# Performance work log

Hardware: AMD Instinct MI355X
Metric: run time of the kernel (lower is better)

Reference implementation:

```python
import jax, jax.numpy as jnp
import numpy as np

N_NODES = 100000


def _graph_conv(x, W, b, src, dst, norm):
    # DGL GraphConv(norm='left'): scale source features by 1/out_degree,
    # aggregate (sum over incoming edges). in_feats > out_feats so weight
    # multiply happens before aggregation (mathematically equivalent either way).
    h = x @ W  # [N, out]
    msg = (h * norm[:, None])[src]  # gather per-edge messages [E, out]
    agg = jax.ops.segment_sum(msg, dst, num_segments=N_NODES)
    return agg + b


def setup_inputs() -> dict:
    key = jax.random.key(0)
    ks = jax.random.split(key, 10)
    in_f, hid_f, out_f = 256, 128, 64
    n_edges = 1_600_000
    feat = jax.random.normal(ks[0], (N_NODES, in_f), dtype=jnp.float32)
    src = jax.random.randint(ks[1], (n_edges,), 0, N_NODES, dtype=jnp.int32)
    dst = jax.random.randint(ks[2], (n_edges,), 0, N_NODES, dtype=jnp.int32)
    noise = jax.random.normal(ks[3], (N_NODES, out_f), dtype=jnp.float32)
    s1 = 1.0 / np.sqrt(in_f)
    s2 = 1.0 / np.sqrt(hid_f)
    W_shared = jax.random.uniform(ks[4], (in_f, hid_f), minval=-s1, maxval=s1, dtype=jnp.float32)
    b_shared = jnp.zeros((hid_f,), jnp.float32)
    W_mu = jax.random.uniform(ks[5], (hid_f, out_f), minval=-s2, maxval=s2, dtype=jnp.float32)
    b_mu = jnp.zeros((out_f,), jnp.float32)
    W_ls = jax.random.uniform(ks[6], (hid_f, out_f), minval=-s2, maxval=s2, dtype=jnp.float32)
    b_ls = jnp.zeros((out_f,), jnp.float32)
    return {"feat": feat, "W_shared": W_shared, "b_shared": b_shared,
            "W_mu": W_mu, "b_mu": b_mu, "W_ls": W_ls, "b_ls": b_ls,
            "noise": noise, "src": src, "dst": dst}


def reference(feat, W_shared, b_shared, W_mu, b_mu, W_ls, b_ls, noise, src, dst):
    # left-norm: 1 / out_degree (clamped to >= 1, as DGL does)
    deg_out = jax.ops.segment_sum(jnp.ones_like(src, jnp.float32), src,
                                  num_segments=N_NODES)
    norm = 1.0 / jnp.maximum(deg_out, 1.0)
    # shared first GraphConv with ReLU activation
    h = jax.nn.relu(_graph_conv(feat, W_shared, b_shared, src, dst, norm))
    # two heads (no activation)
    mu = _graph_conv(h, W_mu, b_mu, src, dst, norm)
    log_sigma = _graph_conv(h, W_ls, b_ls, src, dst, norm)
    # reparameterized sample
    return mu + noise * jnp.exp(log_sigma)
```

## Files before the change

### kernel.cpp

```cpp
#include <hip/hip_runtime.h>
#include <hip/hip_bf16.h>
#include <math.h>

typedef __attribute__((ext_vector_type(8))) short short8;
typedef __attribute__((ext_vector_type(4))) float f32x4;

__device__ __forceinline__ unsigned short f2bf(float f) {
    unsigned int u = __float_as_uint(f);
    u += 0x7FFF + ((u >> 16) & 1);
    return (unsigned short)(u >> 16);
}
__device__ __forceinline__ float b2f(unsigned short s) {
    return __uint_as_float(((unsigned int)s) << 16);
}
__device__ __forceinline__ unsigned int f2bf2(float a, float b) {
    __hip_bfloat162 h = __float22bfloat162_rn(make_float2(a, b));
    return *(unsigned int*)&h;
}

#define EB 8192
#define BSH 10
#define NBKT 128

__global__ __launch_bounds__(256)
void k1_hist(const int* __restrict__ src, const int* __restrict__ dst,
             int* __restrict__ bhist, int E) {
    __shared__ int hist[256];
    int t = threadIdx.x;
    hist[t] = 0;
    __syncthreads();
    int base = blockIdx.x * EB;
    int end = min(base + EB, E);
    for (int e = base + 4 * t; e < end; e += 1024) {
        if (e + 3 < end) {
            int4 d4 = *(const int4*)&dst[e];
            int4 s4 = *(const int4*)&src[e];
            atomicAdd(&hist[d4.x >> BSH], 1);
            atomicAdd(&hist[d4.y >> BSH], 1);
            atomicAdd(&hist[d4.z >> BSH], 1);
            atomicAdd(&hist[d4.w >> BSH], 1);
            atomicAdd(&hist[128 + (s4.x >> BSH)], 1);
            atomicAdd(&hist[128 + (s4.y >> BSH)], 1);
            atomicAdd(&hist[128 + (s4.z >> BSH)], 1);
            atomicAdd(&hist[128 + (s4.w >> BSH)], 1);
        } else {
            for (int q = e; q < end; ++q) {
                atomicAdd(&hist[dst[q] >> BSH], 1);
                atomicAdd(&hist[128 + (src[q] >> BSH)], 1);
            }
        }
    }
    __syncthreads();
    bhist[(size_t)blockIdx.x * 256 + t] = hist[t];
}

__global__ __launch_bounds__(256)
void kc1_totals(const int* __restrict__ bhist, int* __restrict__ totals, int PB) {
    int t = threadIdx.x;
    int slice = (PB + 7) / 8;
    int b0 = blockIdx.x * slice;
    int b1 = min(b0 + slice, PB);
    int s = 0;
    for (int blk = b0; blk < b1; ++blk) s += bhist[(size_t)blk * 256 + t];
    if (s) atomicAdd(&totals[t], s);
}

__global__ __launch_bounds__(256)
void kc2_scan2(const int* __restrict__ totals, int* __restrict__ bbase_d,
               int* __restrict__ bbase_s) {
    __shared__ int s[256];
    int t = threadIdx.x;
    int v = totals[t];
    s[t] = v;
    __syncthreads();
    for (int off = 1; off < 128; off <<= 1) {
        int u = ((t & 127) >= off) ? s[t - off] : 0;
        __syncthreads();
        s[t] += u;
        __syncthreads();
    }
    int excl = s[t] - v;
    if (t < 128) bbase_d[t] = excl;
    else bbase_s[t - 128] = excl;
}

__global__ __launch_bounds__(256)
void kc3_boff(const int* __restrict__ bhist, const int* __restrict__ bbase_d,
              const int* __restrict__ bbase_s, int* __restrict__ boffT, int PB) {
    __shared__ int sums[256];
    int b = blockIdx.x;
    int t = threadIdx.x;
    int v = (t < PB) ? bhist[(size_t)t * 256 + b] : 0;
    sums[t] = v;
    __syncthreads();
    for (int off = 1; off < 256; off <<= 1) {
        int u = (t >= off) ? sums[t - off] : 0;
        __syncthreads();
        sums[t] += u;
        __syncthreads();
    }
    int base = (b < 128) ? bbase_d[b] : bbase_s[b - 128];
    if (t < PB) boffT[(size_t)b * PB + t] = base + sums[t] - v;
}

__global__ __launch_bounds__(256)
void k2_scatter(const int* __restrict__ src, const int* __restrict__ dst,
                const int* __restrict__ boffT, int2* __restrict__ parr,
                int* __restrict__ sarr, int E, int PB) {
    __shared__ int cnt[256];
    int t = threadIdx.x;
    int blk = blockIdx.x;
    cnt[t] = boffT[(size_t)t * PB + blk];
    __syncthreads();
    int base = blk * EB;
    int end = min(base + EB, E);
    for (int e = base + 4 * t; e < end; e += 1024) {
        if (e + 3 < end) {
            int4 s4 = *(const int4*)&src[e];
            int4 d4 = *(const int4*)&dst[e];
            int p0 = atomicAdd(&cnt[d4.x >> BSH], 1); parr[p0] = make_int2(s4.x, d4.x);
            int p1 = atomicAdd(&cnt[d4.y >> BSH], 1); parr[p1] = make_int2(s4.y, d4.y);
            int p2 = atomicAdd(&cnt[d4.z >> BSH], 1); parr[p2] = make_int2(s4.z, d4.z);
            int p3 = atomicAdd(&cnt[d4.w >> BSH], 1); parr[p3] = make_int2(s4.w, d4.w);
            int q0 = atomicAdd(&cnt[128 + (s4.x >> BSH)], 1); sarr[q0] = s4.x;
            int q1 = atomicAdd(&cnt[128 + (s4.y >> BSH)], 1); sarr[q1] = s4.y;
            int q2 = atomicAdd(&cnt[128 + (s4.z >> BSH)], 1); sarr[q2] = s4.z;
            int q3 = atomicAdd(&cnt[128 + (s4.w >> BSH)], 1); sarr[q3] = s4.w;
        } else {
            for (int q = e; q < end; ++q) {
                int sv = src[q], dv = dst[q];
                int pd = atomicAdd(&cnt[dv >> BSH], 1);
                parr[pd] = make_int2(sv, dv);
                int ps = atomicAdd(&cnt[128 + (sv >> BSH)], 1);
                sarr[ps] = sv;
            }
        }
    }
}

__global__ __launch_bounds__(1024)
void k3_dst(const int2* __restrict__ parr, const int* __restrict__ totals,
            const int* __restrict__ bbase_d, int* __restrict__ row_off,
            int* __restrict__ col, int N, int E) {
    __shared__ int hist[1024], sc[1024];
    int b = blockIdx.x, t = threadIdx.x;
    if (b == 0 && t == 0) row_off[N] = E;
    int ne = totals[b];
    int ebase = bbase_d[b];
    hist[t] = 0;
    __syncthreads();
    for (int i = t; i < ne; i += 1024)
        atomicAdd(&hist[parr[ebase + i].y & 1023], 1);
    __syncthreads();
    int h = hist[t];
    sc[t] = h;
    __syncthreads();
    for (int off = 1; off < 1024; off <<= 1) {
        int u = (t >= off) ? sc[t - off] : 0;
        __syncthreads();
        sc[t] += u;
        __syncthreads();
    }
    int excl = sc[t] - h;
    int node = b * 1024 + t;
    if (node < N) row_off[node] = ebase + excl;
    hist[t] = ebase + excl;
    __syncthreads();
    for (int i = t; i < ne; i += 1024) {
        int2 pr = parr[ebase + i];
        int slot = atomicAdd(&hist[pr.y & 1023], 1);
        col[slot] = pr.x;
    }
}

__global__ __launch_bounds__(1024)
void k3_src(const int* __restrict__ sarr, const int* __restrict__ totals_s,
            const int* __restrict__ bbase_s, float* __restrict__ norm, int N) {
    __shared__ int hist[1024];
    int b = blockIdx.x, t = threadIdx.x;
    int ne = totals_s[b];
    int sb = bbase_s[b];
    hist[t] = 0;
    __syncthreads();
    for (int i = t; i < ne; i += 1024)
        atomicAdd(&hist[sarr[sb + i] & 1023], 1);
    __syncthreads();
    int node = b * 1024 + t;
    if (node < N) {
        int d = hist[t];
        norm[node] = 1.0f / (float)(d > 1 ? d : 1);
    }
}

__global__ __launch_bounds__(256)
void k_wprep(const float* __restrict__ Wsh, const float* __restrict__ Wmu,
             const float* __restrict__ Wls, unsigned short* __restrict__ W1T,
             unsigned short* __restrict__ W2T) {
    int b = blockIdx.x, t = threadIdx.x;
    if (b < 128) {
        W1T[(size_t)b * 256 + t] = f2bf(Wsh[(size_t)t * 128 + b]);
    } else {
        int n = b - 128;
        if (t < 128) {
            float v = (n < 64) ? Wmu[(size_t)t * 64 + n]
                               : Wls[(size_t)t * 64 + (n - 64)];
            W2T[(size_t)n * 128 + t] = f2bf(v);
        }
    }
}

__global__ __launch_bounds__(256)
void k_gemm1(const float* __restrict__ A, int M,
             const unsigned short* __restrict__ W1T,
             const float* __restrict__ norm, unsigned short* __restrict__ outb) {
    const int w = threadIdx.x >> 6;
    const int lane = threadIdx.x & 63;
    const int quad = lane >> 4;
    const int l16 = lane & 15;
    const int cl = w * 16 + l16;

    short8 bw[2][8];
#pragma unroll
    for (int hf = 0; hf < 2; ++hf) {
        const unsigned short* wp = W1T + (size_t)(hf * 64 + cl) * 256 + quad * 8;
#pragma unroll
        for (int ks = 0; ks < 8; ++ks)
            bw[hf][ks] = *(const short8*)(wp + ks * 32);
    }

    const int colbase = w * 16 + quad * 4;
    const int r0 = blockIdx.x * 64;

    const float* ap[4];
    int rows[4];
#pragma unroll
    for (int m = 0; m < 4; ++m) {
        int row = r0 + m * 16 + l16;
        rows[m] = row;
        int lr = row < M ? row : M - 1;
        ap[m] = A + (size_t)lr * 256 + quad * 8;
    }
    f32x4 acc[4][2];
#pragma unroll
    for (int m = 0; m < 4; ++m) {
        acc[m][0] = (f32x4){0.f, 0.f, 0.f, 0.f};
        acc[m][1] = (f32x4){0.f, 0.f, 0.f, 0.f};
    }
#pragma unroll
    for (int ks = 0; ks < 8; ++ks) {
#pragma unroll
        for (int m = 0; m < 4; ++m) {
            float4 x = *(const float4*)(ap[m] + ks * 32);
            float4 y = *(const float4*)(ap[m] + ks * 32 + 4);
            union { short8 v; unsigned int u[4]; } c;
            c.u[0] = f2bf2(x.x, x.y);
            c.u[1] = f2bf2(x.z, x.w);
            c.u[2] = f2bf2(y.x, y.y);
            c.u[3] = f2bf2(y.z, y.w);
            acc[m][0] = __builtin_amdgcn_mfma_f32_16x16x32_bf16(bw[0][ks], c.v, acc[m][0], 0, 0, 0);
            acc[m][1] = __builtin_amdgcn_mfma_f32_16x16x32_bf16(bw[1][ks], c.v, acc[m][1], 0, 0, 0);
        }
    }
#pragma unroll
    for (int m = 0; m < 4; ++m) {
        int row = rows[m];
        if (row < M) {
            float nm = norm[row];
            ushort4 o0, o1;
            o0.x = f2bf(acc[m][0][0] * nm); o0.y = f2bf(acc[m][0][1] * nm);
            o0.z = f2bf(acc[m][0][2] * nm); o0.w = f2bf(acc[m][0][3] * nm);
            o1.x = f2bf(acc[m][1][0] * nm); o1.y = f2bf(acc[m][1][1] * nm);
            o1.z = f2bf(acc[m][1][2] * nm); o1.w = f2bf(acc[m][1][3] * nm);
            *(ushort4*)&outb[(size_t)row * 128 + colbase] = o0;
            *(ushort4*)&outb[(size_t)row * 128 + 64 + colbase] = o1;
        }
    }
}

__global__ __launch_bounds__(256)
void k_gemm2(const unsigned short* __restrict__ A, int M,
             const unsigned short* __restrict__ W2T,
             const float* __restrict__ norm, unsigned short* __restrict__ outb) {
    const int w = threadIdx.x >> 6;
    const int lane = threadIdx.x & 63;
    const int quad = lane >> 4;
    const int l16 = lane & 15;
    const int cl = w * 16 + l16;

    short8 bw[2][4];
#pragma unroll
    for (int hf = 0; hf < 2; ++hf) {
        const unsigned short* wp = W2T + (size_t)(hf * 64 + cl) * 128 + quad * 8;
#pragma unroll
        for (int ks = 0; ks < 4; ++ks)
            bw[hf][ks] = *(const short8*)(wp + ks * 32);
    }

    const int colbase = w * 16 + quad * 4;
    const int r0 = blockIdx.x * 64;

    const unsigned short* ap[4];
    int rows[4];
#pragma unroll
    for (int m = 0; m < 4; ++m) {
        int row = r0 + m * 16 + l16;
        rows[m] = row;
        int lr = row < M ? row : M - 1;
        ap[m] = A + (size_t)lr * 128 + quad * 8;
    }
    f32x4 acc[4][2];
#pragma unroll
    for (int m = 0; m < 4; ++m) {
        acc[m][0] = (f32x4){0.f, 0.f, 0.f, 0.f};
        acc[m][1] = (f32x4){0.f, 0.f, 0.f, 0.f};
    }
#pragma unroll
    for (int ks = 0; ks < 4; ++ks) {
#pragma unroll
        for (int m = 0; m < 4; ++m) {
            short8 af = *(const short8*)(ap[m] + ks * 32);
            acc[m][0] = __builtin_amdgcn_mfma_f32_16x16x32_bf16(bw[0][ks], af, acc[m][0], 0, 0, 0);
            acc[m][1] = __builtin_amdgcn_mfma_f32_16x16x32_bf16(bw[1][ks], af, acc[m][1], 0, 0, 0);
        }
    }
#pragma unroll
    for (int m = 0; m < 4; ++m) {
        int row = rows[m];
        if (row < M) {
            float nm = norm[row];
            ushort4 o0, o1;
            o0.x = f2bf(acc[m][0][0] * nm); o0.y = f2bf(acc[m][0][1] * nm);
            o0.z = f2bf(acc[m][0][2] * nm); o0.w = f2bf(acc[m][0][3] * nm);
            o1.x = f2bf(acc[m][1][0] * nm); o1.y = f2bf(acc[m][1][1] * nm);
            o1.z = f2bf(acc[m][1][2] * nm); o1.w = f2bf(acc[m][1][3] * nm);
            *(ushort4*)&outb[(size_t)row * 128 + colbase] = o0;
            *(ushort4*)&outb[(size_t)row * 128 + 64 + colbase] = o1;
        }
    }
}

__global__ __launch_bounds__(256)
void k_spmm_relu(const int* __restrict__ row_off, const int* __restrict__ col,
                 const unsigned short* __restrict__ hxb, const float* __restrict__ bias,
                 unsigned short* __restrict__ hb, int N) {
    int g = (blockIdx.x * blockDim.x + threadIdx.x) >> 5;
    int l = threadIdx.x & 31;
    if (g >= N) return;
    int e0 = row_off[g], e1 = row_off[g + 1];
    const ushort4* base = (const ushort4*)hxb;
    float4 acc = make_float4(0.f, 0.f, 0.f, 0.f);
    int e = e0;
    for (; e + 3 < e1; e += 4) {
        int s0 = col[e], s1 = col[e + 1], s2 = col[e + 2], s3 = col[e + 3];
        ushort4 a = base[(size_t)s0 * 32 + l];
        ushort4 b = base[(size_t)s1 * 32 + l];
        ushort4 c = base[(size_t)s2 * 32 + l];
        ushort4 d = base[(size_t)s3 * 32 + l];
        acc.x += (b2f(a.x) + b2f(b.x)) + (b2f(c.x) + b2f(d.x));
        acc.y += (b2f(a.y) + b2f(b.y)) + (b2f(c.y) + b2f(d.y));
        acc.z += (b2f(a.z) + b2f(b.z)) + (b2f(c.z) + b2f(d.z));
        acc.w += (b2f(a.w) + b2f(b.w)) + (b2f(c.w) + b2f(d.w));
    }
    for (; e < e1; ++e) {
        ushort4 a = base[(size_t)col[e] * 32 + l];
        acc.x += b2f(a.x); acc.y += b2f(a.y); acc.z += b2f(a.z); acc.w += b2f(a.w);
    }
    float4 bi = ((const float4*)bias)[l];
    ushort4 r;
    r.x = f2bf(fmaxf(acc.x + bi.x, 0.f));
    r.y = f2bf(fmaxf(acc.y + bi.y, 0.f));
    r.z = f2bf(fmaxf(acc.z + bi.z, 0.f));
    r.w = f2bf(fmaxf(acc.w + bi.w, 0.f));
    ((ushort4*)hb)[(size_t)g * 32 + l] = r;
}

__global__ __launch_bounds__(256)
void k_spmm_out(const int* __restrict__ row_off, const int* __restrict__ col,
                const unsigned short* __restrict__ hcb, const float* __restrict__ bmu,
                const float* __restrict__ bls, const float* __restrict__ noise,
                float* __restrict__ out, int N) {
    int g = (blockIdx.x * blockDim.x + threadIdx.x) >> 5;
    int l = threadIdx.x & 31;
    if (g >= N) return;
    int e0 = row_off[g], e1 = row_off[g + 1];
    const ushort4* base = (const ushort4*)hcb;
    float4 acc = make_float4(0.f, 0.f, 0.f, 0.f);
    int e = e0;
    for (; e + 3 < e1; e += 4) {
        int s0 = col[e], s1 = col[e + 1], s2 = col[e + 2], s3 = col[e + 3];
        ushort4 a = base[(size_t)s0 * 32 + l];
        ushort4 b = base[(size_t)s1 * 32 + l];
        ushort4 c = base[(size_t)s2 * 32 + l];
        ushort4 d = base[(size_t)s3 * 32 + l];
        acc.x += (b2f(a.x) + b2f(b.x)) + (b2f(c.x) + b2f(d.x));
        acc.y += (b2f(a.y) + b2f(b.y)) + (b2f(c.y) + b2f(d.y));
        acc.z += (b2f(a.z) + b2f(b.z)) + (b2f(c.z) + b2f(d.z));
        acc.w += (b2f(a.w) + b2f(b.w)) + (b2f(c.w) + b2f(d.w));
    }
    for (; e < e1; ++e) {
        ushort4 a = base[(size_t)col[e] * 32 + l];
        acc.x += b2f(a.x); acc.y += b2f(a.y); acc.z += b2f(a.z); acc.w += b2f(a.w);
    }
    int lane64 = threadIdx.x & 63;
    int p = (lane64 + 16) & 63;
    float lx = __shfl(acc.x, p, 64);
    float ly = __shfl(acc.y, p, 64);
    float lz = __shfl(acc.z, p, 64);
    float lw = __shfl(acc.w, p, 64);
    if (l < 16) {
        float4 bm = ((const float4*)bmu)[l];
        float4 bl = ((const float4*)bls)[l];
        float4 nz = ((const float4*)noise)[(size_t)g * 16 + l];
        float4 o;
        o.x = (acc.x + bm.x) + nz.x * expf(lx + bl.x);
        o.y = (acc.y + bm.y) + nz.y * expf(ly + bl.y);
        o.z = (acc.z + bm.z) + nz.z * expf(lz + bl.z);
        o.w = (acc.w + bm.w) + nz.w * expf(lw + bl.w);
        ((float4*)out)[(size_t)g * 16 + l] = o;
    }
}

static inline char* align64(char* p) {
    return (char*)(((uintptr_t)p + 63) & ~(uintptr_t)63);
}

extern "C" void kernel_launch(void* const* d_in, const int* in_sizes, int n_in,
                              void* d_out, int out_size, void* d_ws, size_t ws_size,
                              hipStream_t stream) {
    const float* feat  = (const float*)d_in[0];
    const float* Wsh   = (const float*)d_in[1];
    const float* bsh   = (const float*)d_in[2];
    const float* Wmu   = (const float*)d_in[3];
    const float* bmu   = (const float*)d_in[4];
    const float* Wls   = (const float*)d_in[5];
    const float* bls   = (const float*)d_in[6];
    const float* noise = (const float*)d_in[7];
    const int*   src   = (const int*)d_in[8];
    const int*   dst   = (const int*)d_in[9];
    float* out = (float*)d_out;

    const int N = in_sizes[0] / 256;
    const int E = in_sizes[8];
    const int PB = (E + EB - 1) / EB;

    char* p = (char*)d_ws;
    float* norm   = (float*)p;                  p += (size_t)N * 4;         p = align64(p);
    int* row_off  = (int*)p;                    p += (size_t)(N + 4) * 4;   p = align64(p);
    int* totals   = (int*)p;                    p += 256 * 4;
    int* bbase_d  = (int*)p;                    p += 128 * 4;
    int* bbase_s  = (int*)p;                    p += 128 * 4;               p = align64(p);
    unsigned short* W1T = (unsigned short*)p;   p += (size_t)128 * 256 * 2;
    unsigned short* W2T = (unsigned short*)p;   p += (size_t)128 * 128 * 2;
    p = align64(p);
    int* bhist    = (int*)p;                    p += (size_t)PB * 256 * 4;  p = align64(p);
    int* boffT    = (int*)p;                    p += (size_t)256 * PB * 4;  p = align64(p);
    int2* parr    = (int2*)p;                   p += (size_t)E * 8;
    int* sarr     = (int*)p;                    p += (size_t)E * 4;
    int* col      = (int*)p;                    p += (size_t)E * 4;         p = align64(p);
    unsigned short* hxb = (unsigned short*)p;
    unsigned short* hb  = (unsigned short*)d_out;

    hipMemsetAsync(totals, 0, 256 * sizeof(int), stream);
    k_wprep<<<256, 256, 0, stream>>>(Wsh, Wmu, Wls, W1T, W2T);
    k1_hist<<<PB, 256, 0, stream>>>(src, dst, bhist, E);
    kc1_totals<<<8, 256, 0, stream>>>(bhist, totals, PB);
    kc2_scan2<<<1, 256, 0, stream>>>(totals, bbase_d, bbase_s);
    kc3_boff<<<256, 256, 0, stream>>>(bhist, bbase_d, bbase_s, boffT, PB);
    k2_scatter<<<PB, 256, 0, stream>>>(src, dst, boffT, parr, sarr, E, PB);
    k3_dst<<<NBKT, 1024, 0, stream>>>(parr, totals, bbase_d, row_off, col, N, E);
    k3_src<<<NBKT, 1024, 0, stream>>>(sarr, totals + 128, bbase_s, norm, N);

    int gtiles = (N + 63) / 64;
    k_gemm1<<<gtiles, 256, 0, stream>>>(feat, N, W1T, norm, hxb);
    k_spmm_relu<<<(N * 32 + 255) / 256, 256, 0, stream>>>(row_off, col, hxb, bsh, hb, N);
    k_gemm2<<<gtiles, 256, 0, stream>>>(hb, N, W2T, norm, hxb);
    k_spmm_out<<<(N * 32 + 255) / 256, 256, 0, stream>>>(row_off, col, hxb, bmu, bls, noise, out, N);
}
```

Baseline: 481.3 us.

## Stage GEMM A tiles into LDS via direct global-to-LDS loads; unroll SpMM gathers by 8

Both dense GEMM kernels now copy their 64-row A tile into padded shared memory with global_load_lds 16-byte transfers and a block barrier. The MFMA loop then reads fragments from LDS instead of issuing strided per-lane global loads. The two SpMM kernels unroll the neighbor gather from 4 to 8 edges so more independent loads are in flight, with a 2-edge and 1-edge tail. The cost is a large LDS allocation in gemm1 (about 66 KB), which may limit occupancy, plus an extra synchronization point.

```diff
diff --git a/kernel.cpp b/kernel.cpp
--- a/kernel.cpp
+++ b/kernel.cpp
@@ -16,6 +16,11 @@
 __device__ __forceinline__ unsigned int f2bf2(float a, float b) {
     __hip_bfloat162 h = __float22bfloat162_rn(make_float2(a, b));
     return *(unsigned int*)&h;
+}
+__device__ __forceinline__ void gl_lds16(const void* g, void* l) {
+    __builtin_amdgcn_global_load_lds(
+        (const __attribute__((address_space(1))) void*)g,
+        (__attribute__((address_space(3))) void*)l, 16, 0, 0);
 }
 
 #define EB 8192
@@ -213,11 +218,22 @@
 void k_gemm1(const float* __restrict__ A, int M,
              const unsigned short* __restrict__ W1T,
              const float* __restrict__ norm, unsigned short* __restrict__ outb) {
+    __shared__ char ldsA[64 * 1040];
     const int w = threadIdx.x >> 6;
     const int lane = threadIdx.x & 63;
     const int quad = lane >> 4;
     const int l16 = lane & 15;
     const int cl = w * 16 + l16;
+    const int r0 = blockIdx.x * 64;
+
+#pragma unroll
+    for (int i = 0; i < 16; ++i) {
+        int row = r0 + w * 16 + i;
+        if (row >= M) row = M - 1;
+        const char* g = (const char*)A + (size_t)row * 1024 + lane * 16;
+        char* l = ldsA + (w * 16 + i) * 1040 + lane * 16;
+        gl_lds16(g, l);
+    }
 
     short8 bw[2][8];
 #pragma unroll
@@ -227,19 +243,8 @@
         for (int ks = 0; ks < 8; ++ks)
             bw[hf][ks] = *(const short8*)(wp + ks * 32);
     }
-
-    const int colbase = w * 16 + quad * 4;
-    const int r0 = blockIdx.x * 64;
-
-    const float* ap[4];
-    int rows[4];
-#pragma unroll
-    for (int m = 0; m < 4; ++m) {
-        int row = r0 + m * 16 + l16;
-        rows[m] = row;
-        int lr = row < M ? row : M - 1;
-        ap[m] = A + (size_t)lr * 256 + quad * 8;
-    }
+    __syncthreads();
+
     f32x4 acc[4][2];
 #pragma unroll
     for (int m = 0; m < 4; ++m) {
@@ -250,8 +255,10 @@
     for (int ks = 0; ks < 8; ++ks) {
 #pragma unroll
         for (int m = 0; m < 4; ++m) {
-            float4 x = *(const float4*)(ap[m] + ks * 32);
-            float4 y = *(const float4*)(ap[m] + ks * 32 + 4);
+            const float* pr = (const float*)(ldsA + (m * 16 + l16) * 1040 +
+                                             (ks * 32 + quad * 8) * 4);
+            float4 x = *(const float4*)pr;
+            float4 y = *(const float4*)(pr + 4);
             union { short8 v; unsigned int u[4]; } c;
             c.u[0] = f2bf2(x.x, x.y);
             c.u[1] = f2bf2(x.z, x.w);
@@ -261,9 +268,10 @@
             acc[m][1] = __builtin_amdgcn_mfma_f32_16x16x32_bf16(bw[1][ks], c.v, acc[m][1], 0, 0, 0);
         }
     }
+    const int colbase = w * 16 + quad * 4;
 #pragma unroll
     for (int m = 0; m < 4; ++m) {
-        int row = rows[m];
+        int row = r0 + m * 16 + l16;
         if (row < M) {
             float nm = norm[row];
             ushort4 o0, o1;
@@ -281,11 +289,23 @@
 void k_gemm2(const unsigned short* __restrict__ A, int M,
              const unsigned short* __restrict__ W2T,
              const float* __restrict__ norm, unsigned short* __restrict__ outb) {
+    __shared__ char ldsB[16 * 1040];
     const int w = threadIdx.x >> 6;
     const int lane = threadIdx.x & 63;
     const int quad = lane >> 4;
     const int l16 = lane & 15;
     const int cl = w * 16 + l16;
+    const int r0 = blockIdx.x * 64;
+
+#pragma unroll
+    for (int i = 0; i < 4; ++i) {
+        int c = w * 4 + i;
+        int crow = r0 + c * 4;
+        if (crow + 4 > M) crow = M - 4;
+        const char* g = (const char*)A + (size_t)crow * 256 + lane * 16;
+        char* l = ldsB + c * 1040 + lane * 16;
+        gl_lds16(g, l);
+    }
 
     short8 bw[2][4];
 #pragma unroll
@@ -295,19 +315,8 @@
         for (int ks = 0; ks < 4; ++ks)
             bw[hf][ks] = *(const short8*)(wp + ks * 32);
     }
-
-    const int colbase = w * 16 + quad * 4;
-    const int r0 = blockIdx.x * 64;
-
-    const unsigned short* ap[4];
-    int rows[4];
-#pragma unroll
-    for (int m = 0; m < 4; ++m) {
-        int row = r0 + m * 16 + l16;
-        rows[m] = row;
-        int lr = row < M ? row : M - 1;
-        ap[m] = A + (size_t)lr * 128 + quad * 8;
-    }
+    __syncthreads();
+
     f32x4 acc[4][2];
 #pragma unroll
     for (int m = 0; m < 4; ++m) {
@@ -318,14 +327,17 @@
     for (int ks = 0; ks < 4; ++ks) {
 #pragma unroll
         for (int m = 0; m < 4; ++m) {
-            short8 af = *(const short8*)(ap[m] + ks * 32);
+            int row = m * 16 + l16;
+            short8 af = *(const short8*)(ldsB + (row >> 2) * 1040 + (row & 3) * 256 +
+                                         (ks * 32 + quad * 8) * 2);
             acc[m][0] = __builtin_amdgcn_mfma_f32_16x16x32_bf16(bw[0][ks], af, acc[m][0], 0, 0, 0);
             acc[m][1] = __builtin_amdgcn_mfma_f32_16x16x32_bf16(bw[1][ks], af, acc[m][1], 0, 0, 0);
         }
     }
+    const int colbase = w * 16 + quad * 4;
 #pragma unroll
     for (int m = 0; m < 4; ++m) {
-        int row = rows[m];
+        int row = r0 + m * 16 + l16;
         if (row < M) {
             float nm = norm[row];
             ushort4 o0, o1;
@@ -350,18 +362,33 @@
     const ushort4* base = (const ushort4*)hxb;
     float4 acc = make_float4(0.f, 0.f, 0.f, 0.f);
     int e = e0;
-    for (; e + 3 < e1; e += 4) {
-        int s0 = col[e], s1 = col[e + 1], s2 = col[e + 2], s3 = col[e + 3];
-        ushort4 a = base[(size_t)s0 * 32 + l];
-        ushort4 b = base[(size_t)s1 * 32 + l];
-        ushort4 c = base[(size_t)s2 * 32 + l];
-        ushort4 d = base[(size_t)s3 * 32 + l];
-        acc.x += (b2f(a.x) + b2f(b.x)) + (b2f(c.x) + b2f(d.x));
-        acc.y += (b2f(a.y) + b2f(b.y)) + (b2f(c.y) + b2f(d.y));
-        acc.z += (b2f(a.z) + b2f(b.z)) + (b2f(c.z) + b2f(d.z));
-        acc.w += (b2f(a.w) + b2f(b.w)) + (b2f(c.w) + b2f(d.w));
-    }
-    for (; e < e1; ++e) {
+    for (; e + 7 < e1; e += 8) {
+        ushort4 v0 = base[(size_t)col[e] * 32 + l];
+        ushort4 v1 = base[(size_t)col[e + 1] * 32 + l];
+        ushort4 v2 = base[(size_t)col[e + 2] * 32 + l];
+        ushort4 v3 = base[(size_t)col[e + 3] * 32 + l];
+        ushort4 v4 = base[(size_t)col[e + 4] * 32 + l];
+        ushort4 v5 = base[(size_t)col[e + 5] * 32 + l];
+        ushort4 v6 = base[(size_t)col[e + 6] * 32 + l];
+        ushort4 v7 = base[(size_t)col[e + 7] * 32 + l];
+        acc.x += ((b2f(v0.x) + b2f(v1.x)) + (b2f(v2.x) + b2f(v3.x))) +
+                 ((b2f(v4.x) + b2f(v5.x)) + (b2f(v6.x) + b2f(v7.x)));
+        acc.y += ((b2f(v0.y) + b2f(v1.y)) + (b2f(v2.y) + b2f(v3.y))) +
+                 ((b2f(v4.y) + b2f(v5.y)) + (b2f(v6.y) + b2f(v7.y)));
+        acc.z += ((b2f(v0.z) + b2f(v1.z)) + (b2f(v2.z) + b2f(v3.z))) +
+                 ((b2f(v4.z) + b2f(v5.z)) + (b2f(v6.z) + b2f(v7.z)));
+        acc.w += ((b2f(v0.w) + b2f(v1.w)) + (b2f(v2.w) + b2f(v3.w))) +
+                 ((b2f(v4.w) + b2f(v5.w)) + (b2f(v6.w) + b2f(v7.w)));
+    }
+    for (; e + 1 < e1; e += 2) {
+        ushort4 a = base[(size_t)col[e] * 32 + l];
+        ushort4 b = base[(size_t)col[e + 1] * 32 + l];
+        acc.x += b2f(a.x) + b2f(b.x);
+        acc.y += b2f(a.y) + b2f(b.y);
+        acc.z += b2f(a.z) + b2f(b.z);
+        acc.w += b2f(a.w) + b2f(b.w);
+    }
+    if (e < e1) {
         ushort4 a = base[(size_t)col[e] * 32 + l];
         acc.x += b2f(a.x); acc.y += b2f(a.y); acc.z += b2f(a.z); acc.w += b2f(a.w);
     }
@@ -386,18 +413,33 @@
     const ushort4* base = (const ushort4*)hcb;
     float4 acc = make_float4(0.f, 0.f, 0.f, 0.f);
     int e = e0;
-    for (; e + 3 < e1; e += 4) {
-        int s0 = col[e], s1 = col[e + 1], s2 = col[e + 2], s3 = col[e + 3];
-        ushort4 a = base[(size_t)s0 * 32 + l];
-        ushort4 b = base[(size_t)s1 * 32 + l];
-        ushort4 c = base[(size_t)s2 * 32 + l];
-        ushort4 d = base[(size_t)s3 * 32 + l];
-        acc.x += (b2f(a.x) + b2f(b.x)) + (b2f(c.x) + b2f(d.x));
-        acc.y += (b2f(a.y) + b2f(b.y)) + (b2f(c.y) + b2f(d.y));
-        acc.z += (b2f(a.z) + b2f(b.z)) + (b2f(c.z) + b2f(d.z));
-        acc.w += (b2f(a.w) + b2f(b.w)) + (b2f(c.w) + b2f(d.w));
-    }
-    for (; e < e1; ++e) {
+    for (; e + 7 < e1; e += 8) {
+        ushort4 v0 = base[(size_t)col[e] * 32 + l];
+        ushort4 v1 = base[(size_t)col[e + 1] * 32 + l];
+        ushort4 v2 = base[(size_t)col[e + 2] * 32 + l];
+        ushort4 v3 = base[(size_t)col[e + 3] * 32 + l];
+        ushort4 v4 = base[(size_t)col[e + 4] * 32 + l];
+        ushort4 v5 = base[(size_t)col[e + 5] * 32 + l];
+        ushort4 v6 = base[(size_t)col[e + 6] * 32 + l];
+        ushort4 v7 = base[(size_t)col[e + 7] * 32 + l];
+        acc.x += ((b2f(v0.x) + b2f(v1.x)) + (b2f(v2.x) + b2f(v3.x))) +
+                 ((b2f(v4.x) + b2f(v5.x)) + (b2f(v6.x) + b2f(v7.x)));
+        acc.y += ((b2f(v0.y) + b2f(v1.y)) + (b2f(v2.y) + b2f(v3.y))) +
+                 ((b2f(v4.y) + b2f(v5.y)) + (b2f(v6.y) + b2f(v7.y)));
+        acc.z += ((b2f(v0.z) + b2f(v1.z)) + (b2f(v2.z) + b2f(v3.z))) +
+                 ((b2f(v4.z) + b2f(v5.z)) + (b2f(v6.z) + b2f(v7.z)));
+        acc.w += ((b2f(v0.w) + b2f(v1.w)) + (b2f(v2.w) + b2f(v3.w))) +
+                 ((b2f(v4.w) + b2f(v5.w)) + (b2f(v6.w) + b2f(v7.w)));
+    }
+    for (; e + 1 < e1; e += 2) {
+        ushort4 a = base[(size_t)col[e] * 32 + l];
+        ushort4 b = base[(size_t)col[e + 1] * 32 + l];
+        acc.x += b2f(a.x) + b2f(b.x);
+        acc.y += b2f(a.y) + b2f(b.y);
+        acc.z += b2f(a.z) + b2f(b.z);
+        acc.w += b2f(a.w) + b2f(b.w);
+    }
+    if (e < e1) {
         ushort4 a = base[(size_t)col[e] * 32 + l];
         acc.x += b2f(a.x); acc.y += b2f(a.y); acc.z += b2f(a.z); acc.w += b2f(a.w);
     }
```

After: 450.0 us. -6.5%, faster.
